# Kernel tuning notes

Measured on AMD Instinct MI355X. Metric: run time of the kernel, lower is better.

The kernel has to match this reference:

```python
import jax, jax.numpy as jnp
import numpy as np

NOISE_WEIGHT = 1.0
CHAMFER_WEIGHT = 0.1
CHUNK = 1024


def _min_dist_chunked(a, b):
    """For each point in a [B,N,3], squared distance to nearest point in b [B,M,3].
    Processed in chunks of CHUNK points of `a` to avoid materializing [B,N,M].
    Returns [B,N]."""
    B, N, _ = a.shape
    b_sq = jnp.sum(b * b, axis=-1)  # [B,M]
    nc = N // CHUNK
    a_chunks = jnp.moveaxis(a.reshape(B, nc, CHUNK, 3), 1, 0)  # [nc,B,CHUNK,3]

    def body(carry, a_c):
        a_sq = jnp.sum(a_c * a_c, axis=-1)  # [B,CHUNK]
        # d[b,i,j] = |a_i|^2 + |b_j|^2 - 2 a_i.b_j
        d = a_sq[:, :, None] + b_sq[:, None, :] - 2.0 * jnp.einsum('bid,bjd->bij', a_c, b)
        d = jnp.maximum(d, 0.0)
        return carry, jnp.min(d, axis=2)  # [B,CHUNK]

    _, mins = jax.lax.scan(body, None, a_chunks)  # [nc,B,CHUNK]
    return jnp.moveaxis(mins, 0, 1).reshape(B, N)


def chamfer_distance(pred, target):
    d_pt = _min_dist_chunked(pred, target)   # [B,N]
    d_tp = _min_dist_chunked(target, pred)   # [B,M]
    return jnp.mean(d_pt, axis=1) + jnp.mean(d_tp, axis=1)  # [B]


def setup_inputs() -> dict:
    key = jax.random.key(0)
    k1, k2, k3, k4 = jax.random.split(key, 4)
    B, N = 8, 16384
    return {
        'predicted_noise': jax.random.normal(k1, (B, N, 3), dtype=jnp.float32),
        'actual_noise': jax.random.normal(k2, (B, N, 3), dtype=jnp.float32),
        'predicted_points_coarse': jax.random.normal(k3, (B, N, 3), dtype=jnp.float32),
        'target_points_coarse': jax.random.normal(k4, (B, N, 3), dtype=jnp.float32),
    }


def reference(predicted_noise, actual_noise, predicted_points_coarse, target_points_coarse):
    noise_loss = jnp.mean(jnp.abs(predicted_noise - actual_noise))
    chamfer_loss = jnp.mean(chamfer_distance(predicted_points_coarse, target_points_coarse))
    total_loss = NOISE_WEIGHT * noise_loss + CHAMFER_WEIGHT * chamfer_loss
    return total_loss
```

## Files before the change

kernel.cpp:

```cpp
#include <hip/hip_runtime.h>
#include <stdint.h>

#define NPTS        16384
#define BATCH       8
#define JC          512
#define NCHUNK      (NPTS / JC)
#define QPB         64
#define QBLKS       (NPTS / QPB)
#define CHAM_BLOCKS (BATCH * 2 * QBLKS)
#define NOISE_N     (BATCH * NPTS * 3)
#define NOISE_V4    (NOISE_N / 4)
#define NPTS_TOT    (BATCH * NPTS)
#define PACK_BLOCKS (NPTS_TOT / 256)

#define WS_PK_PRED  0
#define WS_PK_TARG  (8 * NPTS_TOT)

using halfx8 = __attribute__((ext_vector_type(8))) _Float16;
using f32x16 = __attribute__((ext_vector_type(16))) float;
using intx4  = __attribute__((ext_vector_type(4))) int;

__device__ __forceinline__ unsigned int f2h(float f) {
  union { _Float16 h; unsigned short s; } v; v.h = (_Float16)f; return v.s;
}
__device__ __forceinline__ float min3(float a, float b, float c) {
  return fminf(fminf(a, b), c);
}

__device__ __forceinline__ float red33(float m, const f32x16& A, const f32x16& B) {
  float a0 = min3(A[0],  A[1],  A[2]);
  float a1 = min3(A[3],  A[4],  A[5]);
  float a2 = min3(A[6],  A[7],  A[8]);
  float a3 = min3(A[9],  A[10], A[11]);
  float a4 = min3(A[12], A[13], A[14]);
  float b0 = min3(B[0],  B[1],  B[2]);
  float b1 = min3(B[3],  B[4],  B[5]);
  float b2 = min3(B[6],  B[7],  B[8]);
  float b3 = min3(B[9],  B[10], B[11]);
  float b4 = min3(B[12], B[13], B[14]);
  float u0 = min3(a0, a1, a2);
  float u1 = min3(a3, a4, A[15]);
  float v0 = min3(b0, b1, b2);
  float v1 = min3(b3, b4, B[15]);
  float w0 = min3(u0, u1, v0);
  return min3(m, w0, v1);
}

__global__ void pack_noise_kernel(const float* __restrict__ pred,
                                  const float* __restrict__ targ,
                                  const float4* __restrict__ na,
                                  const float4* __restrict__ nb,
                                  ushort4* __restrict__ pk_pred,
                                  ushort4* __restrict__ pk_targ,
                                  float* __restrict__ out) {
  int i = blockIdx.x * 256 + threadIdx.x;
  {
    float x = pred[3*i+0], y = pred[3*i+1], z = pred[3*i+2];
    float s = __builtin_fmaf(x, x, __builtin_fmaf(y, y, z*z));
    pk_pred[i] = make_ushort4((unsigned short)f2h(x), (unsigned short)f2h(y),
                              (unsigned short)f2h(z), (unsigned short)f2h(s));
  }
  {
    float x = targ[3*i+0], y = targ[3*i+1], z = targ[3*i+2];
    float s = __builtin_fmaf(x, x, __builtin_fmaf(y, y, z*z));
    pk_targ[i] = make_ushort4((unsigned short)f2h(x), (unsigned short)f2h(y),
                              (unsigned short)f2h(z), (unsigned short)f2h(s));
  }
  float sn = 0.f;
  if (i < NOISE_V4) {
    float4 pa = na[i], pb = nb[i];
    sn = fabsf(pa.x-pb.x) + fabsf(pa.y-pb.y) + fabsf(pa.z-pb.z) + fabsf(pa.w-pb.w);
  }
  for (int o = 1; o < 64; o <<= 1) sn += __shfl_xor(sn, o);
  __shared__ float ws4[4];
  int lane = threadIdx.x & 63, wv = threadIdx.x >> 6;
  if (lane == 0) ws4[wv] = sn;
  __syncthreads();
  if (threadIdx.x == 0)
    atomicAdd(out, (ws4[0] + ws4[1] + ws4[2] + ws4[3]) * (1.0f / NOISE_N));
}

__global__ __launch_bounds__(128, 6)
void chamfer_kernel(const float* __restrict__ pred_f,
                    const float* __restrict__ targ_f,
                    const ushort4* __restrict__ pk_pred,
                    const ushort4* __restrict__ pk_targ,
                    float* __restrict__ out) {
  __shared__ __align__(16) ushort4 buf[2][JC];
  __shared__ float wsum[2];

  const int tid  = threadIdx.x;
  const int lane = tid & 63;
  const int wv   = tid >> 6;
  const int col  = lane & 31;

  const int blk  = blockIdx.x;
  const int qblk = blk & (QBLKS - 1);
  const int bd   = blk >> 8;
  const int dir  = bd & 1;
  const int b    = bd >> 1;

  const float*   qf  = dir ? targ_f  : pred_f;
  const ushort4* ref = dir ? pk_pred : pk_targ;
  qf += (size_t)b * NPTS * 3; ref += (size_t)b * NPTS;

  const int qg = qblk * QPB + wv * 32 + col;
  float qx = qf[3*qg+0], qy = qf[3*qg+1], qz = qf[3*qg+2];
  float rq = __builtin_fmaf(qx, qx, __builtin_fmaf(qy, qy, qz*qz));
  unsigned int lo = (f2h(-2.f*qy) << 16) | f2h(-2.f*qx);
  unsigned int hi = (0x3C00u << 16) | f2h(-2.f*qz);
  const bool hh = (lane >= 32);

  union BF { halfx8 v; unsigned int u[4]; };
  BF fb0, fb1, fb2, fb3;
  fb0.u[0] = hh ? 0u : lo; fb0.u[1] = hh ? 0u : hi; fb0.u[2] = 0u;           fb0.u[3] = 0u;
  fb1.u[0] = 0u;           fb1.u[1] = 0u;           fb1.u[2] = hh ? 0u : lo; fb1.u[3] = hh ? 0u : hi;
  fb2.u[0] = hh ? lo : 0u; fb2.u[1] = hh ? hi : 0u; fb2.u[2] = 0u;           fb2.u[3] = 0u;
  fb3.u[0] = 0u;           fb3.u[1] = 0u;           fb3.u[2] = hh ? lo : 0u; fb3.u[3] = hh ? hi : 0u;

  f32x16 czero = {0.f,0.f,0.f,0.f, 0.f,0.f,0.f,0.f, 0.f,0.f,0.f,0.f, 0.f,0.f,0.f,0.f};

  auto stage = [&](int c, int pb) {
    size_t go = (size_t)c * (JC * 8) + wv * 2048 + lane * 16;
    const char* g0 = (const char*)ref + go;
    char* l0 = (char*)&buf[pb][0] + wv * 2048 + lane * 16;
    __builtin_amdgcn_global_load_lds(
        (const __attribute__((address_space(1))) unsigned int*)(uintptr_t)g0,
        (__attribute__((address_space(3))) unsigned int*)(unsigned int)(uintptr_t)l0,
        16, 0, 0);
    __builtin_amdgcn_global_load_lds(
        (const __attribute__((address_space(1))) unsigned int*)(uintptr_t)(g0 + 1024),
        (__attribute__((address_space(3))) unsigned int*)(unsigned int)(uintptr_t)(l0 + 1024),
        16, 0, 0);
  };

  stage(0, 0);

  union AF { intx4 i; halfx8 h; };

  float m = 1e30f;
  for (int c = 0; c < NCHUNK; ++c) {
    const int pp = c & 1;
    __syncthreads();
    if (c + 1 < NCHUNK) stage(c + 1, pp ^ 1);
    const char* base = (const char*)&buf[pp][0];
#pragma unroll
    for (int t = 0; t < 4; ++t) {
      AF fa;
      fa.i = *(const intx4*)(base + t * 1024 + lane * 16);
      f32x16 d0 = __builtin_amdgcn_mfma_f32_32x32x16_f16(fa.h, fb0.v, czero, 0, 0, 0);
      f32x16 d1 = __builtin_amdgcn_mfma_f32_32x32x16_f16(fa.h, fb1.v, czero, 0, 0, 0);
      m = red33(m, d0, d1);
      f32x16 d2 = __builtin_amdgcn_mfma_f32_32x32x16_f16(fa.h, fb2.v, czero, 0, 0, 0);
      f32x16 d3 = __builtin_amdgcn_mfma_f32_32x32x16_f16(fa.h, fb3.v, czero, 0, 0, 0);
      m = red33(m, d2, d3);
    }
  }

  m = fminf(m, __shfl_xor(m, 32));
  float dmin = fmaxf(rq + m, 0.f);
  float v = (lane < 32) ? dmin : 0.f;
  for (int o = 1; o < 32; o <<= 1) v += __shfl_xor(v, o);
  if (lane == 0) wsum[wv] = v;
  __syncthreads();
  if (tid == 0)
    atomicAdd(out, (wsum[0] + wsum[1]) * (0.1f / (float)NPTS_TOT));
}

extern "C" void kernel_launch(void* const* d_in, const int* in_sizes, int n_in,
                              void* d_out, int out_size, void* d_ws, size_t ws_size,
                              hipStream_t stream) {
  const float* pn = (const float*)d_in[0];
  const float* an = (const float*)d_in[1];
  const float* pp = (const float*)d_in[2];
  const float* tp = (const float*)d_in[3];

  char* ws = (char*)d_ws;
  ushort4* pk_pred = (ushort4*)(ws + WS_PK_PRED);
  ushort4* pk_targ = (ushort4*)(ws + WS_PK_TARG);
  float*   out     = (float*)d_out;

  hipMemsetAsync(d_out, 0, sizeof(float), stream);
  pack_noise_kernel<<<PACK_BLOCKS, 256, 0, stream>>>(pp, tp, (const float4*)pn,
                                                     (const float4*)an, pk_pred, pk_targ, out);
  chamfer_kernel<<<CHAM_BLOCKS, 128, 0, stream>>>(pp, tp, pk_pred, pk_targ, out);
}
```

Before: 181.0 us.

## Drop LDS staging, give each wave 64 queries, load reference points directly

Removes the double-buffered LDS staging and barriers. Each wave now loads reference fragments straight from global memory with a one-iteration register prefetch. Each wave handles two 32-query groups, so every loaded reference fragment feeds eight MFMAs instead of four. Blocks grow to 256 threads with 256 queries, each wave does its own atomicAdd, and the block-level shared reduction is gone. The trade-off is that the same reference data is fetched by all four waves through L1/L2 rather than shared via LDS, and register pressure rises.

```diff
diff --git a/kernel.cpp b/kernel.cpp
--- a/kernel.cpp
+++ b/kernel.cpp
@@ -3,15 +3,15 @@
 
 #define NPTS        16384
 #define BATCH       8
-#define JC          512
-#define NCHUNK      (NPTS / JC)
-#define QPB         64
+#define QW          64
+#define QPB         256
 #define QBLKS       (NPTS / QPB)
 #define CHAM_BLOCKS (BATCH * 2 * QBLKS)
 #define NOISE_N     (BATCH * NPTS * 3)
 #define NOISE_V4    (NOISE_N / 4)
 #define NPTS_TOT    (BATCH * NPTS)
 #define PACK_BLOCKS (NPTS_TOT / 256)
+#define NITER       (NPTS / 128)
 
 #define WS_PK_PRED  0
 #define WS_PK_TARG  (8 * NPTS_TOT)
@@ -80,15 +80,12 @@
     atomicAdd(out, (ws4[0] + ws4[1] + ws4[2] + ws4[3]) * (1.0f / NOISE_N));
 }
 
-__global__ __launch_bounds__(128, 6)
+__global__ __launch_bounds__(256, 4)
 void chamfer_kernel(const float* __restrict__ pred_f,
                     const float* __restrict__ targ_f,
                     const ushort4* __restrict__ pk_pred,
                     const ushort4* __restrict__ pk_targ,
                     float* __restrict__ out) {
-  __shared__ __align__(16) ushort4 buf[2][JC];
-  __shared__ float wsum[2];
-
   const int tid  = threadIdx.x;
   const int lane = tid & 63;
   const int wv   = tid >> 6;
@@ -96,7 +93,7 @@
 
   const int blk  = blockIdx.x;
   const int qblk = blk & (QBLKS - 1);
-  const int bd   = blk >> 8;
+  const int bd   = blk >> 6;
   const int dir  = bd & 1;
   const int b    = bd >> 1;
 
@@ -104,67 +101,64 @@
   const ushort4* ref = dir ? pk_pred : pk_targ;
   qf += (size_t)b * NPTS * 3; ref += (size_t)b * NPTS;
 
-  const int qg = qblk * QPB + wv * 32 + col;
-  float qx = qf[3*qg+0], qy = qf[3*qg+1], qz = qf[3*qg+2];
-  float rq = __builtin_fmaf(qx, qx, __builtin_fmaf(qy, qy, qz*qz));
-  unsigned int lo = (f2h(-2.f*qy) << 16) | f2h(-2.f*qx);
-  unsigned int hi = (0x3C00u << 16) | f2h(-2.f*qz);
+  const int q0 = qblk * QPB + wv * QW + col;
+  const int q1 = q0 + 32;
+  float q0x = qf[3*q0+0], q0y = qf[3*q0+1], q0z = qf[3*q0+2];
+  float q1x = qf[3*q1+0], q1y = qf[3*q1+1], q1z = qf[3*q1+2];
+  float rq0 = __builtin_fmaf(q0x, q0x, __builtin_fmaf(q0y, q0y, q0z*q0z));
+  float rq1 = __builtin_fmaf(q1x, q1x, __builtin_fmaf(q1y, q1y, q1z*q1z));
+  unsigned int lo0 = (f2h(-2.f*q0y) << 16) | f2h(-2.f*q0x);
+  unsigned int hi0 = (0x3C00u << 16) | f2h(-2.f*q0z);
+  unsigned int lo1 = (f2h(-2.f*q1y) << 16) | f2h(-2.f*q1x);
+  unsigned int hi1 = (0x3C00u << 16) | f2h(-2.f*q1z);
   const bool hh = (lane >= 32);
 
   union BF { halfx8 v; unsigned int u[4]; };
-  BF fb0, fb1, fb2, fb3;
-  fb0.u[0] = hh ? 0u : lo; fb0.u[1] = hh ? 0u : hi; fb0.u[2] = 0u;           fb0.u[3] = 0u;
-  fb1.u[0] = 0u;           fb1.u[1] = 0u;           fb1.u[2] = hh ? 0u : lo; fb1.u[3] = hh ? 0u : hi;
-  fb2.u[0] = hh ? lo : 0u; fb2.u[1] = hh ? hi : 0u; fb2.u[2] = 0u;           fb2.u[3] = 0u;
-  fb3.u[0] = 0u;           fb3.u[1] = 0u;           fb3.u[2] = hh ? lo : 0u; fb3.u[3] = hh ? hi : 0u;
+  BF p0, p1, p2, p3, s0, s1, s2, s3;
+  p0.u[0] = hh ? 0u : lo0; p0.u[1] = hh ? 0u : hi0; p0.u[2] = 0u;            p0.u[3] = 0u;
+  p1.u[0] = 0u;            p1.u[1] = 0u;            p1.u[2] = hh ? 0u : lo0; p1.u[3] = hh ? 0u : hi0;
+  p2.u[0] = hh ? lo0 : 0u; p2.u[1] = hh ? hi0 : 0u; p2.u[2] = 0u;            p2.u[3] = 0u;
+  p3.u[0] = 0u;            p3.u[1] = 0u;            p3.u[2] = hh ? lo0 : 0u; p3.u[3] = hh ? hi0 : 0u;
+  s0.u[0] = hh ? 0u : lo1; s0.u[1] = hh ? 0u : hi1; s0.u[2] = 0u;            s0.u[3] = 0u;
+  s1.u[0] = 0u;            s1.u[1] = 0u;            s1.u[2] = hh ? 0u : lo1; s1.u[3] = hh ? 0u : hi1;
+  s2.u[0] = hh ? lo1 : 0u; s2.u[1] = hh ? hi1 : 0u; s2.u[2] = 0u;            s2.u[3] = 0u;
+  s3.u[0] = 0u;            s3.u[1] = 0u;            s3.u[2] = hh ? lo1 : 0u; s3.u[3] = hh ? hi1 : 0u;
 
   f32x16 czero = {0.f,0.f,0.f,0.f, 0.f,0.f,0.f,0.f, 0.f,0.f,0.f,0.f, 0.f,0.f,0.f,0.f};
 
-  auto stage = [&](int c, int pb) {
-    size_t go = (size_t)c * (JC * 8) + wv * 2048 + lane * 16;
-    const char* g0 = (const char*)ref + go;
-    char* l0 = (char*)&buf[pb][0] + wv * 2048 + lane * 16;
-    __builtin_amdgcn_global_load_lds(
-        (const __attribute__((address_space(1))) unsigned int*)(uintptr_t)g0,
-        (__attribute__((address_space(3))) unsigned int*)(unsigned int)(uintptr_t)l0,
-        16, 0, 0);
-    __builtin_amdgcn_global_load_lds(
-        (const __attribute__((address_space(1))) unsigned int*)(uintptr_t)(g0 + 1024),
-        (__attribute__((address_space(3))) unsigned int*)(unsigned int)(uintptr_t)(l0 + 1024),
-        16, 0, 0);
-  };
+  union AF { intx4 i; halfx8 h; };
+  const intx4* rv = (const intx4*)ref;
 
-  stage(0, 0);
-
-  union AF { intx4 i; halfx8 h; };
-
-  float m = 1e30f;
-  for (int c = 0; c < NCHUNK; ++c) {
-    const int pp = c & 1;
-    __syncthreads();
-    if (c + 1 < NCHUNK) stage(c + 1, pp ^ 1);
-    const char* base = (const char*)&buf[pp][0];
-#pragma unroll
-    for (int t = 0; t < 4; ++t) {
-      AF fa;
-      fa.i = *(const intx4*)(base + t * 1024 + lane * 16);
-      f32x16 d0 = __builtin_amdgcn_mfma_f32_32x32x16_f16(fa.h, fb0.v, czero, 0, 0, 0);
-      f32x16 d1 = __builtin_amdgcn_mfma_f32_32x32x16_f16(fa.h, fb1.v, czero, 0, 0, 0);
-      m = red33(m, d0, d1);
-      f32x16 d2 = __builtin_amdgcn_mfma_f32_32x32x16_f16(fa.h, fb2.v, czero, 0, 0, 0);
-      f32x16 d3 = __builtin_amdgcn_mfma_f32_32x32x16_f16(fa.h, fb3.v, czero, 0, 0, 0);
-      m = red33(m, d2, d3);
-    }
+  float m0 = 1e30f, m1 = 1e30f;
+  AF cur;
+  cur.i = rv[lane];
+#pragma unroll 2
+  for (int t = 0; t < NITER; ++t) {
+    AF nxt;
+    nxt.i = rv[(((t + 1) & (NITER - 1)) << 6) + lane];
+    f32x16 d0 = __builtin_amdgcn_mfma_f32_32x32x16_f16(cur.h, p0.v, czero, 0, 0, 0);
+    f32x16 d1 = __builtin_amdgcn_mfma_f32_32x32x16_f16(cur.h, p1.v, czero, 0, 0, 0);
+    m0 = red33(m0, d0, d1);
+    f32x16 d2 = __builtin_amdgcn_mfma_f32_32x32x16_f16(cur.h, p2.v, czero, 0, 0, 0);
+    f32x16 d3 = __builtin_amdgcn_mfma_f32_32x32x16_f16(cur.h, p3.v, czero, 0, 0, 0);
+    m0 = red33(m0, d2, d3);
+    f32x16 e0 = __builtin_amdgcn_mfma_f32_32x32x16_f16(cur.h, s0.v, czero, 0, 0, 0);
+    f32x16 e1 = __builtin_amdgcn_mfma_f32_32x32x16_f16(cur.h, s1.v, czero, 0, 0, 0);
+    m1 = red33(m1, e0, e1);
+    f32x16 e2 = __builtin_amdgcn_mfma_f32_32x32x16_f16(cur.h, s2.v, czero, 0, 0, 0);
+    f32x16 e3 = __builtin_amdgcn_mfma_f32_32x32x16_f16(cur.h, s3.v, czero, 0, 0, 0);
+    m1 = red33(m1, e2, e3);
+    cur = nxt;
   }
 
-  m = fminf(m, __shfl_xor(m, 32));
-  float dmin = fmaxf(rq + m, 0.f);
-  float v = (lane < 32) ? dmin : 0.f;
-  for (int o = 1; o < 32; o <<= 1) v += __shfl_xor(v, o);
-  if (lane == 0) wsum[wv] = v;
-  __syncthreads();
-  if (tid == 0)
-    atomicAdd(out, (wsum[0] + wsum[1]) * (0.1f / (float)NPTS_TOT));
+  m0 = fminf(m0, __shfl_xor(m0, 32));
+  m1 = fminf(m1, __shfl_xor(m1, 32));
+  float v = 0.f;
+  if (lane < 32)
+    v = fmaxf(rq0 + m0, 0.f) + fmaxf(rq1 + m1, 0.f);
+  for (int o = 1; o < 64; o <<= 1) v += __shfl_xor(v, o);
+  if (lane == 0)
+    atomicAdd(out, v * (0.1f / (float)NPTS_TOT));
 }
 
 extern "C" void kernel_launch(void* const* d_in, const int* in_sizes, int n_in,
@@ -183,5 +177,5 @@
   hipMemsetAsync(d_out, 0, sizeof(float), stream);
   pack_noise_kernel<<<PACK_BLOCKS, 256, 0, stream>>>(pp, tp, (const float4*)pn,
                                                      (const float4*)an, pk_pred, pk_targ, out);
-  chamfer_kernel<<<CHAM_BLOCKS, 128, 0, stream>>>(pp, tp, pk_pred, pk_targ, out);
+  chamfer_kernel<<<CHAM_BLOCKS, 256, 0, stream>>>(pp, tp, pk_pred, pk_targ, out);
 }
```

After: 200.3 us. 10.7% more time.

## Double queries per block and issue paired MFMAs via inline asm

Applied to the files above, without the earlier changes.

Each chamfer block now holds 128 query points in four waves instead of 64 in two. The shared reference chunk loaded into LDS is therefore reused by twice as many queries, and each wave issues one global-to-LDS load per stage instead of two. The MFMA pairs are written in inline assembly with fixed s_nop padding, which hard-codes the hazard waits and may block the compiler from interleaving the min-reduction with the MFMAs. Halving the block count also coarsens the grid.

```diff
diff --git a/kernel.cpp b/kernel.cpp
--- a/kernel.cpp
+++ b/kernel.cpp
@@ -5,7 +5,7 @@
 #define BATCH       8
 #define JC          512
 #define NCHUNK      (NPTS / JC)
-#define QPB         64
+#define QPB         128
 #define QBLKS       (NPTS / QPB)
 #define CHAM_BLOCKS (BATCH * 2 * QBLKS)
 #define NOISE_N     (BATCH * NPTS * 3)
@@ -26,6 +26,16 @@
 __device__ __forceinline__ float min3(float a, float b, float c) {
   return fminf(fminf(a, b), c);
 }
+
+#define MFMA2(D0, D1, A, B0, B1, C)                              \
+  asm volatile("s_nop 1\n\t"                                     \
+               "v_mfma_f32_32x32x16_f16 %0, %2, %3, %5\n\t"      \
+               "v_mfma_f32_32x32x16_f16 %1, %2, %4, %5\n\t"      \
+               "s_nop 7\n\t"                                     \
+               "s_nop 7\n\t"                                     \
+               "s_nop 4"                                         \
+               : "=&v"(D0), "=&v"(D1)                            \
+               : "v"(A), "v"(B0), "v"(B1), "v"(C))
 
 __device__ __forceinline__ float red33(float m, const f32x16& A, const f32x16& B) {
   float a0 = min3(A[0],  A[1],  A[2]);
@@ -80,14 +90,14 @@
     atomicAdd(out, (ws4[0] + ws4[1] + ws4[2] + ws4[3]) * (1.0f / NOISE_N));
 }
 
-__global__ __launch_bounds__(128, 6)
+__global__ __launch_bounds__(256, 4)
 void chamfer_kernel(const float* __restrict__ pred_f,
                     const float* __restrict__ targ_f,
                     const ushort4* __restrict__ pk_pred,
                     const ushort4* __restrict__ pk_targ,
                     float* __restrict__ out) {
   __shared__ __align__(16) ushort4 buf[2][JC];
-  __shared__ float wsum[2];
+  __shared__ float wsum[4];
 
   const int tid  = threadIdx.x;
   const int lane = tid & 63;
@@ -96,7 +106,7 @@
 
   const int blk  = blockIdx.x;
   const int qblk = blk & (QBLKS - 1);
-  const int bd   = blk >> 8;
+  const int bd   = blk >> 7;
   const int dir  = bd & 1;
   const int b    = bd >> 1;
 
@@ -104,8 +114,8 @@
   const ushort4* ref = dir ? pk_pred : pk_targ;
   qf += (size_t)b * NPTS * 3; ref += (size_t)b * NPTS;
 
-  const int qg = qblk * QPB + wv * 32 + col;
-  float qx = qf[3*qg+0], qy = qf[3*qg+1], qz = qf[3*qg+2];
+  const int q = qblk * QPB + wv * 32 + col;
+  float qx = qf[3*q+0], qy = qf[3*q+1], qz = qf[3*q+2];
   float rq = __builtin_fmaf(qx, qx, __builtin_fmaf(qy, qy, qz*qz));
   unsigned int lo = (f2h(-2.f*qy) << 16) | f2h(-2.f*qx);
   unsigned int hi = (0x3C00u << 16) | f2h(-2.f*qz);
@@ -121,16 +131,11 @@
   f32x16 czero = {0.f,0.f,0.f,0.f, 0.f,0.f,0.f,0.f, 0.f,0.f,0.f,0.f, 0.f,0.f,0.f,0.f};
 
   auto stage = [&](int c, int pb) {
-    size_t go = (size_t)c * (JC * 8) + wv * 2048 + lane * 16;
-    const char* g0 = (const char*)ref + go;
-    char* l0 = (char*)&buf[pb][0] + wv * 2048 + lane * 16;
+    const char* g = (const char*)ref + (size_t)c * (JC * 8) + wv * 1024 + lane * 16;
+    char* l = (char*)&buf[pb][0] + wv * 1024 + lane * 16;
     __builtin_amdgcn_global_load_lds(
-        (const __attribute__((address_space(1))) unsigned int*)(uintptr_t)g0,
-        (__attribute__((address_space(3))) unsigned int*)(unsigned int)(uintptr_t)l0,
-        16, 0, 0);
-    __builtin_amdgcn_global_load_lds(
-        (const __attribute__((address_space(1))) unsigned int*)(uintptr_t)(g0 + 1024),
-        (__attribute__((address_space(3))) unsigned int*)(unsigned int)(uintptr_t)(l0 + 1024),
+        (const __attribute__((address_space(1))) unsigned int*)(uintptr_t)g,
+        (__attribute__((address_space(3))) unsigned int*)(unsigned int)(uintptr_t)l,
         16, 0, 0);
   };
 
@@ -148,12 +153,11 @@
     for (int t = 0; t < 4; ++t) {
       AF fa;
       fa.i = *(const intx4*)(base + t * 1024 + lane * 16);
-      f32x16 d0 = __builtin_amdgcn_mfma_f32_32x32x16_f16(fa.h, fb0.v, czero, 0, 0, 0);
-      f32x16 d1 = __builtin_amdgcn_mfma_f32_32x32x16_f16(fa.h, fb1.v, czero, 0, 0, 0);
+      f32x16 d0, d1;
+      MFMA2(d0, d1, fa.h, fb0.v, fb1.v, czero);
       m = red33(m, d0, d1);
-      f32x16 d2 = __builtin_amdgcn_mfma_f32_32x32x16_f16(fa.h, fb2.v, czero, 0, 0, 0);
-      f32x16 d3 = __builtin_amdgcn_mfma_f32_32x32x16_f16(fa.h, fb3.v, czero, 0, 0, 0);
-      m = red33(m, d2, d3);
+      MFMA2(d0, d1, fa.h, fb2.v, fb3.v, czero);
+      m = red33(m, d0, d1);
     }
   }
 
@@ -164,7 +168,7 @@
   if (lane == 0) wsum[wv] = v;
   __syncthreads();
   if (tid == 0)
-    atomicAdd(out, (wsum[0] + wsum[1]) * (0.1f / (float)NPTS_TOT));
+    atomicAdd(out, (wsum[0] + wsum[1] + wsum[2] + wsum[3]) * (0.1f / (float)NPTS_TOT));
 }
 
 extern "C" void kernel_launch(void* const* d_in, const int* in_sizes, int n_in,
@@ -183,5 +187,5 @@
   hipMemsetAsync(d_out, 0, sizeof(float), stream);
   pack_noise_kernel<<<PACK_BLOCKS, 256, 0, stream>>>(pp, tp, (const float4*)pn,
                                                      (const float4*)an, pk_pred, pk_targ, out);
-  chamfer_kernel<<<CHAM_BLOCKS, 128, 0, stream>>>(pp, tp, pk_pred, pk_targ, out);
+  chamfer_kernel<<<CHAM_BLOCKS, 256, 0, stream>>>(pp, tp, pk_pred, pk_targ, out);
 }
```

After: 185.0 us. 2.2% more time.
